# Kernel tuning notes

Measured on AMD Instinct MI355X. Metric: run time of the kernel, lower is better.

## Reference

```python
import jax, jax.numpy as jnp
import numpy as np

B, S, IN, H = 64, 64, 512, 512  # batch, seq(=n_unit), in_dim, out_dim


def setup_inputs() -> dict:
    key = jax.random.key(0)
    k1, k2, k3 = jax.random.split(key, 3)
    x = jax.random.normal(k1, (B, S, IN), dtype=jnp.float32)
    # one distinct LSTM cell per timestep (units[i] used at step i), bias=False
    # gate order follows torch.nn.LSTMCell: i, f, g, o
    W_ih = jax.random.normal(k2, (S, 4 * H, IN), dtype=jnp.float32) * 0.02
    W_hh = jax.random.normal(k3, (S, 4 * H, H), dtype=jnp.float32) * 0.02
    return {"x": x, "W_ih": W_ih, "W_hh": W_hh}


def reference(x, W_ih, W_hh):
    b, s, _ = x.shape
    h_dim = W_hh.shape[-1]
    xs = jnp.swapaxes(x, 0, 1)  # [S, B, IN]

    def step(carry, inp):
        h, c = carry
        xt, wih, whh = inp  # [B,IN], [4H,IN], [4H,H]
        gates = xt @ wih.T + h @ whh.T  # [B, 4H]
        i, f, g, o = jnp.split(gates, 4, axis=-1)
        i = jax.nn.sigmoid(i)
        f = jax.nn.sigmoid(f)
        g = jnp.tanh(g)
        o = jax.nn.sigmoid(o)
        c = f * c + i * g
        h = o * jnp.tanh(c)
        return (h, c), h

    h0 = jnp.zeros((b, h_dim), dtype=x.dtype)  # step 0 gets None state -> zeros
    c0 = jnp.zeros((b, h_dim), dtype=x.dtype)
    _, hs = jax.lax.scan(step, (h0, c0), (xs, W_ih, W_hh))  # hs: [S, B, H]
    return jnp.swapaxes(hs, 0, 1)  # [B, S, H]
```

## Files before the change

kernel.cpp:

```cpp
#include <hip/hip_runtime.h>


#define NWG  256
#define NTHR 512

constexpr int S  = 64;
constexpr int NB = 64;
constexpr int IN = 512;
constexpr int H  = 512;
constexpr int BH = NB * H;
constexpr int RING = 8;

typedef __attribute__((ext_vector_type(8))) short bf16x8;
typedef __attribute__((ext_vector_type(4))) float fx4;

__device__ __forceinline__ short to_bf16(float f) {
  union { float f; unsigned u; } v; v.f = f;
  unsigned r = (v.u + 0x7fffu + ((v.u >> 16) & 1u)) >> 16;
  return (short)r;
}
__device__ __forceinline__ bf16x8 cvt8(fx4 a, fx4 b) {
  bf16x8 r;
  r[0] = to_bf16(a[0]); r[1] = to_bf16(a[1]); r[2] = to_bf16(a[2]); r[3] = to_bf16(a[3]);
  r[4] = to_bf16(b[0]); r[5] = to_bf16(b[1]); r[6] = to_bf16(b[2]); r[7] = to_bf16(b[3]);
  return r;
}
__device__ __forceinline__ fx4 ld_h4(const float* p) {
  union { unsigned long long u[2]; fx4 f; } v;
  const unsigned long long* q = (const unsigned long long*)p;
  v.u[0] = __hip_atomic_load(q,     __ATOMIC_RELAXED, __HIP_MEMORY_SCOPE_AGENT);
  v.u[1] = __hip_atomic_load(q + 1, __ATOMIC_RELAXED, __HIP_MEMORY_SCOPE_AGENT);
  return v.f;
}
__device__ __forceinline__ float sigm(float x) { return 1.0f / (1.0f + __expf(-x)); }
__device__ __forceinline__ float tanh_f(float x) { return 2.0f / (1.0f + __expf(-2.0f * x)) - 1.0f; }

__device__ __forceinline__ int lds_ld(const int* p) {
  return __hip_atomic_load(p, __ATOMIC_RELAXED, __HIP_MEMORY_SCOPE_WORKGROUP);
}
__device__ __forceinline__ void lds_st(int* p, int v) {
  __hip_atomic_store(p, v, __ATOMIC_RELAXED, __HIP_MEMORY_SCOPE_WORKGROUP);
}

__global__ void init_flags(int* flags) {
  flags[blockIdx.x * blockDim.x + threadIdx.x] = 0;
}

__global__ void __launch_bounds__(NTHR, 2) lstm_fused(
    const float* __restrict__ x, const float* __restrict__ Wih,
    const float* __restrict__ Whh, float* __restrict__ out,
    float* __restrict__ hbuf, int* __restrict__ flags)
{
  __shared__ float xring[RING * 4 * 512];
  __shared__ float redh[2 * 4 * 512];
  __shared__ int xfill[4];
  __shared__ int hfill[4];
  __shared__ int sfill[2];
  __shared__ int go_seq;
  __shared__ int cons_seq;

  const int wg   = blockIdx.x;
  const int tid  = threadIdx.x;
  const int wave = tid >> 6;
  const int lane = tid & 63;
  const int cc   = lane & 15;
  const int quad = lane >> 4;
  const int mhalf = wg & 1;
  const int n0    = (wg >> 1) << 2;
  const int jrow  = ((cc >> 2) << 9) + n0 + (cc & 3);
  const int b0    = (mhalf << 5) + cc;
  const int b1    = b0 + 16;
  const int kq    = ((wave & 3) << 7) + (quad << 3);
  const int rloc  = (quad << 6) + cc;

  if (tid < 4) { xfill[tid] = 0; hfill[tid] = 0; }
  if (tid < 2) { sfill[tid] = 0; }
  if (tid == 0) { go_seq = 0; cons_seq = 0; }
  __syncthreads();

  if (wave < 4) {
    const float* wrow = Wih + (size_t)jrow * IN + kq;
    const float* xr0  = x + (size_t)b0 * (S * IN) + kq;
    const float* xr1  = x + (size_t)b1 * (S * IN) + kq;
    fx4 wA[8], wB[8];
    auto load_w = [&](fx4 (&w)[8], int tt) {
      const float* wp = wrow + ((size_t)tt << 20);
#pragma unroll
      for (int s2 = 0; s2 < 4; ++s2) {
        w[2 * s2]     = *(const fx4*)(wp + (s2 << 5));
        w[2 * s2 + 1] = *(const fx4*)(wp + (s2 << 5) + 4);
      }
    };
    load_w(wA, 0);

    auto pstep = [&](int t, fx4 (&wc)[8], fx4 (&wn)[8]) {
      if (t + 1 < S) load_w(wn, t + 1);
      if (t >= RING) {
        while (lds_ld(&cons_seq) < t - RING + 1) __builtin_amdgcn_s_sleep(1);
        __asm__ volatile("" ::: "memory");
      }
      fx4 acc0 = {0.f, 0.f, 0.f, 0.f}, acc1 = {0.f, 0.f, 0.f, 0.f};
      const float* a0 = xr0 + t * IN;
      const float* a1 = xr1 + t * IN;
#pragma unroll
      for (int s2 = 0; s2 < 4; ++s2) {
        bf16x8 wf  = cvt8(wc[2 * s2], wc[2 * s2 + 1]);
        bf16x8 af0 = cvt8(*(const fx4*)(a0 + (s2 << 5)), *(const fx4*)(a0 + (s2 << 5) + 4));
        bf16x8 af1 = cvt8(*(const fx4*)(a1 + (s2 << 5)), *(const fx4*)(a1 + (s2 << 5) + 4));
        acc0 = __builtin_amdgcn_mfma_f32_16x16x32_bf16(af0, wf, acc0, 0, 0, 0);
        acc1 = __builtin_amdgcn_mfma_f32_16x16x32_bf16(af1, wf, acc1, 0, 0, 0);
      }
      float* dst = xring + ((t & (RING - 1)) << 11) + (wave << 9) + rloc;
#pragma unroll
      for (int r = 0; r < 4; ++r) {
        dst[r << 4]         = acc0[r];
        dst[(r << 4) + 256] = acc1[r];
      }
      __asm__ volatile("s_waitcnt lgkmcnt(0)" ::: "memory");
      if (lane == 0) lds_st(&xfill[wave], t + 1);
    };
#pragma unroll 1
    for (int t = 0; t < S; t += 2) { pstep(t, wA, wB); pstep(t + 1, wB, wA); }

  } else {
    const float* wrow = Whh + (size_t)jrow * IN + kq;
    const float* hr0  = hbuf + (size_t)b0 * H + kq;
    const float* hr1  = hbuf + (size_t)b1 * H + kq;
    const int w4 = wave - 4;
    const int ct = tid - 256;
    const int cm = ct >> 2, cn = ct & 3;
    const int ob = (mhalf << 5) + cm, ocol = n0 + cn;
    const bool is_cell = (ct < 128);
    float c_state = 0.f;

    fx4 wA[8], wB[8];
    auto load_w = [&](fx4 (&w)[8], int tt) {
      const float* wp = wrow + ((size_t)tt << 20);
#pragma unroll
      for (int s2 = 0; s2 < 4; ++s2) {
        w[2 * s2]     = *(const fx4*)(wp + (s2 << 5));
        w[2 * s2 + 1] = *(const fx4*)(wp + (s2 << 5) + 4);
      }
    };

    auto cstep = [&](int t, fx4 (&wc)[8], fx4 (&wn)[8]) {
      if (t + 1 < S) load_w(wn, t + 1);
      fx4 acc0 = {0.f, 0.f, 0.f, 0.f}, acc1 = {0.f, 0.f, 0.f, 0.f};
      if (t > 0) {
        if (wave == 7) {
          const int* fl = flags + ((t - 1) << 8) + mhalf;
          while (true) {
            int f0 = __hip_atomic_load(fl + (lane << 1),        __ATOMIC_RELAXED, __HIP_MEMORY_SCOPE_AGENT);
            int f1 = __hip_atomic_load(fl + ((lane + 64) << 1), __ATOMIC_RELAXED, __HIP_MEMORY_SCOPE_AGENT);
            if (__ballot((f0 & f1) != 0) == ~0ull) break;
            __builtin_amdgcn_s_sleep(2);
          }
          __asm__ volatile("" ::: "memory");
          if (lane == 0) lds_st(&go_seq, t);
        } else {
          while (lds_ld(&go_seq) < t) __builtin_amdgcn_s_sleep(1);
          __asm__ volatile("" ::: "memory");
        }
        const float* h0 = hr0 + (size_t)(t & 1) * BH;
        const float* h1 = hr1 + (size_t)(t & 1) * BH;
#pragma unroll
        for (int s2 = 0; s2 < 4; ++s2) {
          bf16x8 wf  = cvt8(wc[2 * s2], wc[2 * s2 + 1]);
          bf16x8 af0 = cvt8(ld_h4(h0 + (s2 << 5)), ld_h4(h0 + (s2 << 5) + 4));
          bf16x8 af1 = cvt8(ld_h4(h1 + (s2 << 5)), ld_h4(h1 + (s2 << 5) + 4));
          acc0 = __builtin_amdgcn_mfma_f32_16x16x32_bf16(af0, wf, acc0, 0, 0, 0);
          acc1 = __builtin_amdgcn_mfma_f32_16x16x32_bf16(af1, wf, acc1, 0, 0, 0);
        }
      }
      if (t >= 2) {
        while (lds_ld(&cons_seq) < t - 1) __builtin_amdgcn_s_sleep(1);
        __asm__ volatile("" ::: "memory");
      }
      float* dst = redh + ((t & 1) << 11) + (w4 << 9) + rloc;
#pragma unroll
      for (int r = 0; r < 4; ++r) {
        dst[r << 4]         = acc0[r];
        dst[(r << 4) + 256] = acc1[r];
      }
      __asm__ volatile("s_waitcnt lgkmcnt(0)" ::: "memory");
      if (lane == 0) lds_st(&hfill[w4], t + 1);

      if (is_cell) {
        for (;;) {
          bool ok = true;
#pragma unroll
          for (int w = 0; w < 4; ++w) {
            ok &= lds_ld(&xfill[w]) >= t + 1;
            ok &= lds_ld(&hfill[w]) >= t + 1;
          }
          if (ok) break;
          __builtin_amdgcn_s_sleep(1);
        }
        __asm__ volatile("" ::: "memory");
        const float* xs = xring + ((t & (RING - 1)) << 11);
        const float* hs = redh + ((t & 1) << 11);
        const int o = (cm << 4) + cn;
        float gv[4];
#pragma unroll
        for (int g = 0; g < 4; ++g) {
          float s = 0.f;
          const int oo = o + (g << 2);
#pragma unroll
          for (int w = 0; w < 4; ++w)
            s += xs[(w << 9) + oo] + hs[(w << 9) + oo];
          gv[g] = s;
        }
        float ig = sigm(gv[0]);
        float fg = sigm(gv[1]);
        float gg = tanh_f(gv[2]);
        float og = sigm(gv[3]);
        c_state  = fg * c_state + ig * gg;
        float h  = og * tanh_f(c_state);
        out[((size_t)ob * S + t) * H + ocol] = h;
        __hip_atomic_store(hbuf + (size_t)((t + 1) & 1) * BH + (size_t)ob * H + ocol,
                           h, __ATOMIC_RELAXED, __HIP_MEMORY_SCOPE_AGENT);
        __asm__ volatile("s_waitcnt vmcnt(0)" ::: "memory");
        if (lane == 0) lds_st(&sfill[w4], t + 1);
        if (tid == 256) {
          while (lds_ld(&sfill[1]) < t + 1) __builtin_amdgcn_s_sleep(1);
          __hip_atomic_store(flags + (t << 8) + wg, 1, __ATOMIC_RELAXED, __HIP_MEMORY_SCOPE_AGENT);
          lds_st(&cons_seq, t + 1);
        }
      }
    };
#pragma unroll 1
    for (int t = 0; t < S; t += 2) { cstep(t, wA, wB); cstep(t + 1, wB, wA); }
  }
}

extern "C" void kernel_launch(void* const* d_in, const int* in_sizes, int n_in,
                              void* d_out, int out_size, void* d_ws, size_t ws_size,
                              hipStream_t stream) {
  const float* x   = (const float*)d_in[0];
  const float* Wih = (const float*)d_in[1];
  const float* Whh = (const float*)d_in[2];
  float* out = (float*)d_out;

  float* hbuf = (float*)d_ws;
  int* flags  = (int*)((char*)d_ws + (size_t)2 * BH * sizeof(float));

  hipLaunchKernelGGL(init_flags, dim3(64), dim3(256), 0, stream, flags);
  hipLaunchKernelGGL(lstm_fused, dim3(NWG), dim3(NTHR), 0, stream,
                     x, Wih, Whh, out, hbuf, flags);
}
```

Measured before the change: 1.098 ms.

## Replace per-workgroup flag polling with grouped atomic counters and pad LDS rows

The cross-workgroup barrier that gates each timestep's recurrent matmul is rebuilt. Each workgroup now atomically increments one of 8 counters per (step, batch half) instead of writing its own flag. Every consumer wave polls just 8 counters directly, replacing the old scheme where one wave scanned 128 flags and relayed the result through LDS. Separately, the LDS staging buffers for partial gate sums get a row pitch of 17 floats to reduce bank conflicts. Atomic contention on each counter (16 increments) and every wave polling global memory may add traffic.

```diff
diff --git a/kernel.cpp b/kernel.cpp
--- a/kernel.cpp
+++ b/kernel.cpp
@@ -10,6 +10,9 @@
 constexpr int H  = 512;
 constexpr int BH = NB * H;
 constexpr int RING = 8;
+constexpr int ROWP = 17;
+constexpr int SLAB = 32 * ROWP;
+constexpr int SLOT = 4 * SLAB;
 
 typedef __attribute__((ext_vector_type(8))) short bf16x8;
 typedef __attribute__((ext_vector_type(4))) float fx4;
@@ -49,14 +52,13 @@
 __global__ void __launch_bounds__(NTHR, 2) lstm_fused(
     const float* __restrict__ x, const float* __restrict__ Wih,
     const float* __restrict__ Whh, float* __restrict__ out,
-    float* __restrict__ hbuf, int* __restrict__ flags)
+    float* __restrict__ hbuf, int* __restrict__ cnt)
 {
-  __shared__ float xring[RING * 4 * 512];
-  __shared__ float redh[2 * 4 * 512];
+  __shared__ float xring[RING * SLOT];
+  __shared__ float redh[2 * SLOT];
   __shared__ int xfill[4];
   __shared__ int hfill[4];
   __shared__ int sfill[2];
-  __shared__ int go_seq;
   __shared__ int cons_seq;
 
   const int wg   = blockIdx.x;
@@ -67,15 +69,16 @@
   const int quad = lane >> 4;
   const int mhalf = wg & 1;
   const int n0    = (wg >> 1) << 2;
+  const int xgrp  = (wg >> 1) & 7;
   const int jrow  = ((cc >> 2) << 9) + n0 + (cc & 3);
   const int b0    = (mhalf << 5) + cc;
   const int b1    = b0 + 16;
   const int kq    = ((wave & 3) << 7) + (quad << 3);
-  const int rloc  = (quad << 6) + cc;
+  const int rloc  = quad * (4 * ROWP) + cc;
 
   if (tid < 4) { xfill[tid] = 0; hfill[tid] = 0; }
   if (tid < 2) { sfill[tid] = 0; }
-  if (tid == 0) { go_seq = 0; cons_seq = 0; }
+  if (tid == 0) { cons_seq = 0; }
   __syncthreads();
 
   if (wave < 4) {
@@ -110,11 +113,11 @@
         acc0 = __builtin_amdgcn_mfma_f32_16x16x32_bf16(af0, wf, acc0, 0, 0, 0);
         acc1 = __builtin_amdgcn_mfma_f32_16x16x32_bf16(af1, wf, acc1, 0, 0, 0);
       }
-      float* dst = xring + ((t & (RING - 1)) << 11) + (wave << 9) + rloc;
+      float* dst = xring + (t & (RING - 1)) * SLOT + wave * SLAB + rloc;
 #pragma unroll
       for (int r = 0; r < 4; ++r) {
-        dst[r << 4]         = acc0[r];
-        dst[(r << 4) + 256] = acc1[r];
+        dst[r * ROWP]             = acc0[r];
+        dst[r * ROWP + 16 * ROWP] = acc1[r];
       }
       __asm__ volatile("s_waitcnt lgkmcnt(0)" ::: "memory");
       if (lane == 0) lds_st(&xfill[wave], t + 1);
@@ -147,20 +150,15 @@
       if (t + 1 < S) load_w(wn, t + 1);
       fx4 acc0 = {0.f, 0.f, 0.f, 0.f}, acc1 = {0.f, 0.f, 0.f, 0.f};
       if (t > 0) {
-        if (wave == 7) {
-          const int* fl = flags + ((t - 1) << 8) + mhalf;
-          while (true) {
-            int f0 = __hip_atomic_load(fl + (lane << 1),        __ATOMIC_RELAXED, __HIP_MEMORY_SCOPE_AGENT);
-            int f1 = __hip_atomic_load(fl + ((lane + 64) << 1), __ATOMIC_RELAXED, __HIP_MEMORY_SCOPE_AGENT);
-            if (__ballot((f0 & f1) != 0) == ~0ull) break;
-            __builtin_amdgcn_s_sleep(2);
-          }
-          __asm__ volatile("" ::: "memory");
-          if (lane == 0) lds_st(&go_seq, t);
-        } else {
-          while (lds_ld(&go_seq) < t) __builtin_amdgcn_s_sleep(1);
-          __asm__ volatile("" ::: "memory");
-        }
+        const int* cp = cnt + (((t - 1) << 1) + mhalf) * 8;
+        while (true) {
+          int c = (lane < 8)
+            ? __hip_atomic_load(cp + lane, __ATOMIC_RELAXED, __HIP_MEMORY_SCOPE_AGENT)
+            : 16;
+          if (__ballot(c == 16) == ~0ull) break;
+          __builtin_amdgcn_s_sleep(1);
+        }
+        __asm__ volatile("" ::: "memory");
         const float* h0 = hr0 + (size_t)(t & 1) * BH;
         const float* h1 = hr1 + (size_t)(t & 1) * BH;
 #pragma unroll
@@ -176,11 +174,11 @@
         while (lds_ld(&cons_seq) < t - 1) __builtin_amdgcn_s_sleep(1);
         __asm__ volatile("" ::: "memory");
       }
-      float* dst = redh + ((t & 1) << 11) + (w4 << 9) + rloc;
+      float* dst = redh + (t & 1) * SLOT + w4 * SLAB + rloc;
 #pragma unroll
       for (int r = 0; r < 4; ++r) {
-        dst[r << 4]         = acc0[r];
-        dst[(r << 4) + 256] = acc1[r];
+        dst[r * ROWP]             = acc0[r];
+        dst[r * ROWP + 16 * ROWP] = acc1[r];
       }
       __asm__ volatile("s_waitcnt lgkmcnt(0)" ::: "memory");
       if (lane == 0) lds_st(&hfill[w4], t + 1);
@@ -197,9 +195,9 @@
           __builtin_amdgcn_s_sleep(1);
         }
         __asm__ volatile("" ::: "memory");
-        const float* xs = xring + ((t & (RING - 1)) << 11);
-        const float* hs = redh + ((t & 1) << 11);
-        const int o = (cm << 4) + cn;
+        const float* xs = xring + (t & (RING - 1)) * SLOT;
+        const float* hs = redh + (t & 1) * SLOT;
+        const int o = cm * ROWP + cn;
         float gv[4];
 #pragma unroll
         for (int g = 0; g < 4; ++g) {
@@ -207,7 +205,7 @@
           const int oo = o + (g << 2);
 #pragma unroll
           for (int w = 0; w < 4; ++w)
-            s += xs[(w << 9) + oo] + hs[(w << 9) + oo];
+            s += xs[w * SLAB + oo] + hs[w * SLAB + oo];
           gv[g] = s;
         }
         float ig = sigm(gv[0]);
@@ -223,7 +221,8 @@
         if (lane == 0) lds_st(&sfill[w4], t + 1);
         if (tid == 256) {
           while (lds_ld(&sfill[1]) < t + 1) __builtin_amdgcn_s_sleep(1);
-          __hip_atomic_store(flags + (t << 8) + wg, 1, __ATOMIC_RELAXED, __HIP_MEMORY_SCOPE_AGENT);
+          __hip_atomic_fetch_add(cnt + ((t << 1) + mhalf) * 8 + xgrp, 1,
+                                 __ATOMIC_RELAXED, __HIP_MEMORY_SCOPE_AGENT);
           lds_st(&cons_seq, t + 1);
         }
       }
@@ -242,9 +241,9 @@
   float* out = (float*)d_out;
 
   float* hbuf = (float*)d_ws;
-  int* flags  = (int*)((char*)d_ws + (size_t)2 * BH * sizeof(float));
-
-  hipLaunchKernelGGL(init_flags, dim3(64), dim3(256), 0, stream, flags);
+  int* cnt    = (int*)((char*)d_ws + (size_t)2 * BH * sizeof(float));
+
+  hipLaunchKernelGGL(init_flags, dim3(64), dim3(256), 0, stream, cnt);
   hipLaunchKernelGGL(lstm_fused, dim3(NWG), dim3(NTHR), 0, stream,
-                     x, Wih, Whh, out, hbuf, flags);
-}
+                     x, Wih, Whh, out, hbuf, cnt);
+}
```

New measurement: 1.656 ms. +50.8%, slower.
